# Optimization experiments

Measured on AMD Instinct MI355X. Metric: run time of the kernel, lower is better.

Reference implementation:

```python
import jax, jax.numpy as jnp
import numpy as np

N, E, G = 50000, 800000, 64
IN, ED = 2, 2
H1, C1 = 16, 8
H2, C2 = 4, 16
D1 = H1 * C1  # 128
D2 = H2 * C2  # 64


def _glorot(key, shape):
    fan_in, fan_out = shape[0], shape[-1]
    lim = jnp.sqrt(6.0 / (fan_in + fan_out))
    return jax.random.uniform(key, shape, jnp.float32, -lim, lim)


def setup_inputs() -> dict:
    key = jax.random.key(0)
    ks = jax.random.split(key, 16)
    x = jax.random.normal(ks[0], (N, IN), jnp.float32)
    edge_attr = jax.random.uniform(ks[1], (E, ED), jnp.float32)
    edge_index = jax.random.randint(ks[2], (2, E), 0, N, jnp.int64)
    batch = jnp.sort(jax.random.randint(ks[3], (N,), 0, G, jnp.int64))
    return {
        'x': x, 'edge_attr': edge_attr,
        'W_l1': _glorot(ks[4], (IN, D1)), 'b_l1': jnp.zeros((D1,), jnp.float32),
        'W_r1': _glorot(ks[5], (IN, D1)), 'b_r1': jnp.zeros((D1,), jnp.float32),
        'W_e1': _glorot(ks[6], (ED, D1)),
        'att1': _glorot(ks[7], (H1, C1)),
        'bias1': jnp.zeros((D1,), jnp.float32),
        'W_l2': _glorot(ks[8], (D1, D2)), 'b_l2': jnp.zeros((D2,), jnp.float32),
        'W_r2': _glorot(ks[9], (D1, D2)), 'b_r2': jnp.zeros((D2,), jnp.float32),
        'W_e2': _glorot(ks[10], (ED, D2)),
        'att2': _glorot(ks[11], (H2, C2)),
        'bias2': jnp.zeros((D2,), jnp.float32),
        'edge_index': edge_index, 'batch': batch,
    }


def _gatv2(x, edge_attr, src, tgt, Wl, bl, Wr, br, We, att, bias, H, C):
    n = x.shape[0]
    xl = (x @ Wl + bl).reshape(n, H, C)          # source transform (lin_l)
    xr = (x @ Wr + br).reshape(n, H, C)          # target transform (lin_r)
    xe = (edge_attr @ We).reshape(-1, H, C)      # edge transform (no bias)
    m = xl[src] + xr[tgt] + xe                   # [E,H,C]
    e = jnp.einsum('ehc,hc->eh', jax.nn.leaky_relu(m, 0.2), att)  # [E,H]
    emax = jax.ops.segment_max(e, tgt, num_segments=n)
    ee = jnp.exp(e - emax[tgt])
    denom = jax.ops.segment_sum(ee, tgt, num_segments=n)
    alpha = ee / denom[tgt]                      # segment softmax over in-edges
    out = jax.ops.segment_sum(alpha[:, :, None] * xl[src], tgt, num_segments=n)
    return out.reshape(n, H * C) + bias


def reference(x, edge_attr, W_l1, b_l1, W_r1, b_r1, W_e1, att1, bias1,
              W_l2, b_l2, W_r2, b_r2, W_e2, att2, bias2, edge_index, batch):
    src, tgt = edge_index[0], edge_index[1]
    h = _gatv2(x, edge_attr, src, tgt, W_l1, b_l1, W_r1, b_r1, W_e1, att1, bias1, H1, C1)
    h = jax.nn.elu(h)  # dropout is identity in eval mode
    h = _gatv2(h, edge_attr, src, tgt, W_l2, b_l2, W_r2, b_r2, W_e2, att2, bias2, H2, C2)
    # global_mean_pool over graphs
    sums = jax.ops.segment_sum(h, batch, num_segments=G)
    cnts = jax.ops.segment_sum(jnp.ones((h.shape[0], 1), h.dtype), batch, num_segments=G)
    return sums / jnp.maximum(cnts, 1.0)
```

## Files before the change

kernel.cpp:

```cpp
#include <hip/hip_runtime.h>
#include <math.h>

#define NBLK 256


template<int CTRL>
__device__ __forceinline__ float dppf(float x) {
    return __int_as_float(__builtin_amdgcn_update_dpp(
        0, __float_as_int(x), CTRL, 0xF, 0xF, true));
}
__device__ __forceinline__ float quadsum(float x) {
    x += dppf<0xB1>(x);
    x += dppf<0x4E>(x);
    return x;
}
__device__ __forceinline__ float sum16(float x) {
    x += dppf<0xB1>(x);
    x += dppf<0x4E>(x);
    x += dppf<0x141>(x);
    x += dppf<0x140>(x);
    return x;
}


__global__ __launch_bounds__(256) void k_hist(const int* __restrict__ tgt,
                                              int* __restrict__ gh,
                                              int e, int chunk, int nbuck) {
    __shared__ int lh[256];
    int tid = threadIdx.x, blk = blockIdx.x;
    lh[tid] = 0;
    __syncthreads();
    int lo = blk * chunk, hi = min(lo + chunk, e);
    for (int i = lo + tid; i < hi; i += 256)
        atomicAdd(&lh[tgt[i] >> 8], 1);
    __syncthreads();
    if (tid < nbuck) gh[tid * NBLK + blk] = lh[tid];
}


__global__ __launch_bounds__(256) void k_scanA(const int* __restrict__ deg,
                                               int* __restrict__ excl,
                                               int* __restrict__ bsum, int n) {
    int i = blockIdx.x * 256 + threadIdx.x;
    int lane = threadIdx.x & 63, wv = threadIdx.x >> 6;
    int v = (i < n) ? deg[i] : 0;
    int incl = v;
#pragma unroll
    for (int off = 1; off < 64; off <<= 1) {
        int t = __shfl_up(incl, off);
        if (lane >= off) incl += t;
    }
    __shared__ int ws[4];
    if (lane == 63) ws[wv] = incl;
    __syncthreads();
    int prefix = 0;
    for (int k = 0; k < wv; ++k) prefix += ws[k];
    if (i < n) excl[i] = prefix + incl - v;
    if (threadIdx.x == 255) bsum[blockIdx.x] = prefix + incl;
}

__global__ __launch_bounds__(256) void k_scanB(const int* __restrict__ bsum, int* __restrict__ boff,
                                               int* __restrict__ total_at, int nb, int n) {
    __shared__ int ws[4];
    __shared__ int carry_s;
    int lane = threadIdx.x & 63, wv = threadIdx.x >> 6;
    if (threadIdx.x == 0) carry_s = 0;
    __syncthreads();
    for (int base = 0; base < nb; base += 256) {
        int i = base + threadIdx.x;
        int v = (i < nb) ? bsum[i] : 0;
        int incl = v;
#pragma unroll
        for (int off = 1; off < 64; off <<= 1) {
            int t = __shfl_up(incl, off);
            if (lane >= off) incl += t;
        }
        if (lane == 63) ws[wv] = incl;
        __syncthreads();
        int prefix = carry_s;
        for (int k = 0; k < wv; ++k) prefix += ws[k];
        if (i < nb) boff[i] = prefix + incl - v;
        __syncthreads();
        if (threadIdx.x == 255) carry_s = prefix + incl;
        __syncthreads();
    }
    if (threadIdx.x == 0) total_at[n] = carry_s;
}

__global__ void k_scanC(int* __restrict__ arr, const int* __restrict__ boff, int n) {
    int i = blockIdx.x * 256 + threadIdx.x;
    if (i < n) arr[i] += boff[blockIdx.x];
}


__global__ __launch_bounds__(256) void k_binplace(const int* __restrict__ src,
                                                  const int* __restrict__ tgt,
                                                  const float* __restrict__ ea,
                                                  const float* __restrict__ x,
                                                  const int* __restrict__ gexcl,
                                                  float4* __restrict__ brec,
                                                  int* __restrict__ bmeta,
                                                  int e, int chunk, int nbuck) {
    __shared__ int loff[256];
    int tid = threadIdx.x, blk = blockIdx.x;
    if (tid < nbuck) loff[tid] = gexcl[tid * NBLK + blk];
    __syncthreads();
    int lo = blk * chunk, hi = min(lo + chunk, e);
    for (int i = lo + tid; i < hi; i += 256) {
        int t = tgt[i], s = src[i];
        float2 ev = ((const float2*)ea)[i];
        float2 xv = *(const float2*)(x + 2 * (size_t)s);
        int dst = atomicAdd(&loff[t >> 8], 1);
        brec[dst] = make_float4(xv.x, xv.y, ev.x, ev.y);
        bmeta[dst] = (s & 0xFFFF) | ((t & 0xFF) << 16);
    }
}


__global__ __launch_bounds__(256) void k_place2(const int* __restrict__ gexcl,
                                                const int* __restrict__ bmeta,
                                                const float4* __restrict__ brec,
                                                float4* __restrict__ col_rec,
                                                int* __restrict__ col_src,
                                                int* __restrict__ rowp, int n) {
    __shared__ int hist[256];
    __shared__ int pos[256];
    __shared__ int ws[4];
    int b = blockIdx.x, tid = threadIdx.x;
    int lo = gexcl[b * NBLK], hi = gexcl[(b + 1) * NBLK];
    hist[tid] = 0;
    __syncthreads();
    for (int i = lo + tid; i < hi; i += 256)
        atomicAdd(&hist[(bmeta[i] >> 16) & 0xFF], 1);
    __syncthreads();
    int lane = tid & 63, wv = tid >> 6;
    int v = hist[tid];
    int incl = v;
#pragma unroll
    for (int off = 1; off < 64; off <<= 1) {
        int t = __shfl_up(incl, off);
        if (lane >= off) incl += t;
    }
    if (lane == 63) ws[wv] = incl;
    __syncthreads();
    int prefix = 0;
    for (int k = 0; k < wv; ++k) prefix += ws[k];
    int rp = lo + prefix + incl - v;
    int node = b * 256 + tid;
    if (node <= n) rowp[node] = rp;
    if (b == (int)gridDim.x - 1 && tid == 0) rowp[n] = hi;
    pos[tid] = rp;
    __syncthreads();
    for (int i = lo + tid; i < hi; i += 256) {
        int m = bmeta[i];
        float4 r = brec[i];
        int slot = atomicAdd(&pos[(m >> 16) & 0xFF], 1);
        col_rec[slot] = r;
        col_src[slot] = m & 0xFFFF;
    }
}


__global__ __launch_bounds__(256) void k_agg1(
    const float* __restrict__ x,
    const int* __restrict__ rowp,
    const float4* __restrict__ col_rec,
    const float* __restrict__ W_l1, const float* __restrict__ b_l1,
    const float* __restrict__ W_r1, const float* __restrict__ b_r1,
    const float* __restrict__ W_e1,
    const float* __restrict__ att1,
    const float* __restrict__ bias1,
    float* __restrict__ hpost,
    int n)
{
    int wid = (blockIdx.x * blockDim.x + threadIdx.x) >> 6;
    if (wid >= n) return;
    int v = __builtin_amdgcn_readfirstlane(wid);
    int lane = threadIdx.x & 63;
    int f0 = 2 * lane, f1 = 2 * lane + 1;

    float Wl00 = W_l1[f0], Wl10 = W_l1[128 + f0], bl0 = b_l1[f0];
    float Wl01 = W_l1[f1], Wl11 = W_l1[128 + f1], bl1 = b_l1[f1];
    float We00 = W_e1[f0], We10 = W_e1[128 + f0];
    float We01 = W_e1[f1], We11 = W_e1[128 + f1];
    float a0 = att1[f0], a1 = att1[f1];

    float xv0 = x[2 * v], xv1 = x[2 * v + 1];
    float xrA = xv0 * W_r1[f0] + xv1 * W_r1[128 + f0] + b_r1[f0];
    float xrB = xv0 * W_r1[f1] + xv1 * W_r1[128 + f1] + b_r1[f1];

    float lh = 0.f, acc0 = 0.f, acc1 = 0.f;
    int rs = rowp[v], re = rowp[v + 1];
    bool b0 = (lane & 1) != 0, b1 = (lane & 2) != 0;

    int cs = rs;
#define E1(K, R) \
    float xa##K = fmaf(R.x, Wl00, fmaf(R.y, Wl10, bl0)); \
    float xb##K = fmaf(R.x, Wl01, fmaf(R.y, Wl11, bl1)); \
    float s##K; { \
        float m0 = xa##K + xrA + R.z * We00 + R.w * We10; \
        float m1 = xb##K + xrB + R.z * We01 + R.w * We11; \
        s##K = quadsum(fmaf(fmaxf(m0, 0.2f * m0), a0, fmaxf(m1, 0.2f * m1) * a1)); \
    }
    for (; cs + 4 <= re; cs += 4) {
        float4 r0 = col_rec[cs + 0];
        float4 r1 = col_rec[cs + 1];
        float4 r2 = col_rec[cs + 2];
        float4 r3 = col_rec[cs + 3];
        E1(0, r0) E1(1, r1) E1(2, r2) E1(3, r3)
        float sel01 = b0 ? s1 : s0;
        float sel23 = b0 ? s3 : s2;
        float smy = b1 ? sel23 : sel01;
        float p = __expf(smy);
        float p0 = dppf<0x00>(p), p1 = dppf<0x55>(p), p2 = dppf<0xAA>(p), p3 = dppf<0xFF>(p);
        lh += (p0 + p1) + (p2 + p3);
        acc0 += fmaf(p0, xa0, p1 * xa1) + fmaf(p2, xa2, p3 * xa3);
        acc1 += fmaf(p0, xb0, p1 * xb1) + fmaf(p2, xb2, p3 * xb3);
    }
#undef E1
    for (; cs < re; ++cs) {
        float4 r = col_rec[cs];
        float xa = fmaf(r.x, Wl00, fmaf(r.y, Wl10, bl0));
        float xb = fmaf(r.x, Wl01, fmaf(r.y, Wl11, bl1));
        float m0 = xa + xrA + r.z * We00 + r.w * We10;
        float m1 = xb + xrB + r.z * We01 + r.w * We11;
        float s = quadsum(fmaf(fmaxf(m0, 0.2f * m0), a0, fmaxf(m1, 0.2f * m1) * a1));
        float p = __expf(s);
        lh += p;
        acc0 = fmaf(p, xa, acc0);
        acc1 = fmaf(p, xb, acc1);
    }

    float r0o, r1o;
    if (re > rs) { float inv = 1.f / lh; r0o = acc0 * inv; r1o = acc1 * inv; }
    else { r0o = 0.f; r1o = 0.f; }
    r0o += bias1[f0]; r1o += bias1[f1];
    r0o = (r0o > 0.f) ? r0o : (__expf(r0o) - 1.f);
    r1o = (r1o > 0.f) ? r1o : (__expf(r1o) - 1.f);
    *(float2*)(hpost + (size_t)v * 128 + f0) = make_float2(r0o, r1o);
}


struct XF2Shared {
    float4 hs[64 * 32];
    float4 ws[128 * 16];
};

__device__ __forceinline__ void xf2_pass(XF2Shared& sm,
                                         const float* __restrict__ W,
                                         const float* __restrict__ b,
                                         float* __restrict__ out,
                                         int v0, int n, int t) {
    __syncthreads();
    {
        const float4* wsrc = (const float4*)W;
#pragma unroll
        for (int i = 0; i < 8; ++i) sm.ws[t + 256 * i] = wsrc[t + 256 * i];
    }
    __syncthreads();

    int lane = t & 63, w = t >> 6;
    int fg = lane & 3, ng = lane >> 2;
    int fq = 4 * w + fg;
    int hsw = ng & 7;

    float acc[4][4];
#pragma unroll
    for (int i = 0; i < 4; ++i)
#pragma unroll
        for (int c = 0; c < 4; ++c) acc[i][c] = 0.f;

    for (int kq = 0; kq < 32; ++kq) {
        float4 w0 = sm.ws[(4 * kq + 0) * 16 + fq];
        float4 w1 = sm.ws[(4 * kq + 1) * 16 + fq];
        float4 w2 = sm.ws[(4 * kq + 2) * 16 + fq];
        float4 w3 = sm.ws[(4 * kq + 3) * 16 + fq];
        int ks = kq ^ hsw;
        float4 h0 = sm.hs[(4 * ng + 0) * 32 + ks];
        float4 h1 = sm.hs[(4 * ng + 1) * 32 + ks];
        float4 h2 = sm.hs[(4 * ng + 2) * 32 + ks];
        float4 h3 = sm.hs[(4 * ng + 3) * 32 + ks];
#pragma unroll
        for (int i = 0; i < 4; ++i) {
            float4 h = (i == 0) ? h0 : (i == 1) ? h1 : (i == 2) ? h2 : h3;
            acc[i][0] += h.x * w0.x; acc[i][1] += h.x * w0.y; acc[i][2] += h.x * w0.z; acc[i][3] += h.x * w0.w;
            acc[i][0] += h.y * w1.x; acc[i][1] += h.y * w1.y; acc[i][2] += h.y * w1.z; acc[i][3] += h.y * w1.w;
            acc[i][0] += h.z * w2.x; acc[i][1] += h.z * w2.y; acc[i][2] += h.z * w2.z; acc[i][3] += h.z * w2.w;
            acc[i][0] += h.w * w3.x; acc[i][1] += h.w * w3.y; acc[i][2] += h.w * w3.z; acc[i][3] += h.w * w3.w;
        }
    }

    float4 bf = ((const float4*)b)[fq];
#pragma unroll
    for (int i = 0; i < 4; ++i) {
        int node = v0 + 4 * ng + i;
        if (node < n) {
            float4 r = make_float4(acc[i][0] + bf.x, acc[i][1] + bf.y,
                                   acc[i][2] + bf.z, acc[i][3] + bf.w);
            *(float4*)(out + (size_t)node * 64 + 4 * fq) = r;
        }
    }
}

__global__ __launch_bounds__(256) void k_transform2(
    const float* __restrict__ hpost,
    const float* __restrict__ W_l2, const float* __restrict__ b_l2,
    const float* __restrict__ W_r2, const float* __restrict__ b_r2,
    float* __restrict__ xl2, float* __restrict__ xr2, int n)
{
    __shared__ XF2Shared sm;
    int t = threadIdx.x;
    int v0 = blockIdx.x * 64;
    {
        int node = t >> 2, sub = t & 3;
        int sw = (node >> 2) & 7;
        bool valid = (v0 + node) < n;
        const float4* src = (const float4*)(hpost + (size_t)(v0 + node) * 128);
#pragma unroll
        for (int i = 0; i < 8; ++i) {
            int kq = sub + 4 * i;
            float4 val = valid ? src[kq] : make_float4(0.f, 0.f, 0.f, 0.f);
            sm.hs[node * 32 + (kq ^ sw)] = val;
        }
    }
    xf2_pass(sm, W_l2, b_l2, xl2, v0, n, t);
    xf2_pass(sm, W_r2, b_r2, xr2, v0, n, t);
}


__global__ __launch_bounds__(256) void k_agg2(
    const float* __restrict__ xl2,
    const float* __restrict__ xr2,
    const int* __restrict__ rowp,
    const int* __restrict__ col_src,
    const float4* __restrict__ col_rec,
    const float* __restrict__ W_e2,
    const float* __restrict__ att2,
    const float* __restrict__ bias2,
    float* __restrict__ h2,
    int n)
{
    int wid = (blockIdx.x * blockDim.x + threadIdx.x) >> 6;
    if (wid >= n) return;
    int v = __builtin_amdgcn_readfirstlane(wid);
    int lane = threadIdx.x & 63;
    float We0 = W_e2[lane], We1 = W_e2[64 + lane];
    float a = att2[lane];
    float xr = xr2[(size_t)v * 64 + lane];
    float lh = 0.f, acc = 0.f;
    int rs = rowp[v], re = rowp[v + 1];
    const float2* eap = (const float2*)col_rec;
    bool b0 = (lane & 1) != 0, b1 = (lane & 2) != 0;

    int cs = rs;
#define E2(K, EV, XL) \
    float s##K; { \
        float m = XL + xr + EV.x * We0 + EV.y * We1; \
        s##K = sum16(fmaxf(m, 0.2f * m) * a); \
    }
    for (; cs + 4 <= re; cs += 4) {
        int u0 = col_src[cs], u1 = col_src[cs + 1], u2 = col_src[cs + 2], u3 = col_src[cs + 3];
        float2 e0 = eap[2 * cs + 1], e1 = eap[2 * cs + 3];
        float2 e2 = eap[2 * cs + 5], e3 = eap[2 * cs + 7];
        float xl0 = xl2[(size_t)u0 * 64 + lane];
        float xl1 = xl2[(size_t)u1 * 64 + lane];
        float xl2_ = xl2[(size_t)u2 * 64 + lane];
        float xl3 = xl2[(size_t)u3 * 64 + lane];
        E2(0, e0, xl0) E2(1, e1, xl1) E2(2, e2, xl2_) E2(3, e3, xl3)
        float sel01 = b0 ? s1 : s0;
        float sel23 = b0 ? s3 : s2;
        float smy = b1 ? sel23 : sel01;
        float p = __expf(smy);
        float p0 = dppf<0x00>(p), p1 = dppf<0x55>(p), p2 = dppf<0xAA>(p), p3 = dppf<0xFF>(p);
        lh += (p0 + p1) + (p2 + p3);
        acc += fmaf(p0, xl0, p1 * xl1) + fmaf(p2, xl2_, p3 * xl3);
    }
#undef E2
    for (; cs < re; ++cs) {
        int u = col_src[cs];
        float2 ev = eap[2 * cs + 1];
        float xl = xl2[(size_t)u * 64 + lane];
        float m = xl + xr + ev.x * We0 + ev.y * We1;
        float s = sum16(fmaxf(m, 0.2f * m) * a);
        float p = __expf(s);
        lh += p;
        acc = fmaf(p, xl, acc);
    }
    float r = (re > rs) ? acc / lh : 0.f;
    h2[(size_t)v * 64 + lane] = r + bias2[lane];
}


__global__ __launch_bounds__(256) void k_pool2(const float* __restrict__ h2,
                                               const int* __restrict__ batch,
                                               float* __restrict__ sums, float* __restrict__ cnt,
                                               int n, int chunk) {
    int w = (blockIdx.x * blockDim.x + threadIdx.x) >> 6;
    int lane = threadIdx.x & 63;
    int start = w * chunk;
    if (start >= n) return;
    int end = min(n, start + chunk);
    int g = batch[start];
    float acc = 0.f;
    int c = 0;
    for (int v = start; v < end; ++v) {
        int bg = batch[v];
        if (bg != g) {
            atomicAdd(&sums[g * 64 + lane], acc);
            if (lane == 0) atomicAdd(&cnt[g], (float)c);
            acc = 0.f; c = 0; g = bg;
        }
        acc += h2[(size_t)v * 64 + lane];
        ++c;
    }
    atomicAdd(&sums[g * 64 + lane], acc);
    if (lane == 0) atomicAdd(&cnt[g], (float)c);
}

__global__ void k_final(const float* __restrict__ sums, const float* __restrict__ cnt,
                        float* __restrict__ out, int g) {
    int i = blockIdx.x * blockDim.x + threadIdx.x;
    if (i < g * 64) out[i] = sums[i] / fmaxf(cnt[i >> 6], 1.f);
}


extern "C" void kernel_launch(void* const* d_in, const int* in_sizes, int n_in,
                              void* d_out, int out_size, void* d_ws, size_t ws_size,
                              hipStream_t stream) {
    const float* x     = (const float*)d_in[0];
    const float* ea    = (const float*)d_in[1];
    const float* W_l1  = (const float*)d_in[2];
    const float* b_l1  = (const float*)d_in[3];
    const float* W_r1  = (const float*)d_in[4];
    const float* b_r1  = (const float*)d_in[5];
    const float* W_e1  = (const float*)d_in[6];
    const float* att1  = (const float*)d_in[7];
    const float* bias1 = (const float*)d_in[8];
    const float* W_l2  = (const float*)d_in[9];
    const float* b_l2  = (const float*)d_in[10];
    const float* W_r2  = (const float*)d_in[11];
    const float* b_r2  = (const float*)d_in[12];
    const float* W_e2  = (const float*)d_in[13];
    const float* att2  = (const float*)d_in[14];
    const float* bias2 = (const float*)d_in[15];
    const int* eidx    = (const int*)d_in[16];
    const int* batch   = (const int*)d_in[17];

    int n = in_sizes[0] / 2;
    int e = in_sizes[16] / 2;
    int g = out_size / 64;
    const int* srcI = eidx;
    const int* tgtI = eidx + e;
    int nb = (n + 255) / 256;
    int ntot = nb * NBLK;
    int nb2 = (ntot + 255) / 256;
    int chunk = (e + NBLK - 1) / NBLK;

    char* w = (char*)d_ws;
    size_t off = 0;
    auto take = [&](size_t bytes) -> char* {
        size_t a = (off + 255) & ~(size_t)255;
        off = a + bytes;
        return w + a;
    };
    char*   reg1    = take((size_t)n * 128 * 4);
    float4* brec    = (float4*)reg1;
    float*  hpost   = (float*)reg1;
    float*  h2      = hpost;
    char*   reg2    = take((size_t)n * 64 * 4);
    int*    bmeta   = (int*)reg2;
    float*  xl2     = (float*)reg2;

    float*  xr2     = (float*)take((size_t)n * 64 * 4);
    float4* col_rec = (float4*)take((size_t)e * 16);
    int*    col_src = (int*)take((size_t)e * 4);
    int*    rowp    = (int*)take((size_t)(n + 1) * 4);
    int*    gh      = (int*)take((size_t)ntot * 4);
    int*    gexcl   = (int*)take((size_t)(ntot + 1) * 4);
    int*    gbsum   = (int*)take((size_t)nb2 * 4);
    int*    gboff   = (int*)take((size_t)nb2 * 4);
    float*  sums    = (float*)take((size_t)g * 64 * 4);
    float*  cnt     = (float*)take((size_t)g * 4);

    hipMemsetAsync(sums, 0, (size_t)g * 64 * 4, stream);
    hipMemsetAsync(cnt, 0, (size_t)g * 4, stream);

    k_hist<<<NBLK, 256, 0, stream>>>(tgtI, gh, e, chunk, nb);
    k_scanA<<<nb2, 256, 0, stream>>>(gh, gexcl, gbsum, ntot);
    k_scanB<<<1, 256, 0, stream>>>(gbsum, gboff, gexcl, nb2, ntot);
    k_scanC<<<nb2, 256, 0, stream>>>(gexcl, gboff, ntot);
    k_binplace<<<NBLK, 256, 0, stream>>>(srcI, tgtI, ea, x, gexcl, brec, bmeta, e, chunk, nb);
    k_place2<<<nb, 256, 0, stream>>>(gexcl, bmeta, brec, col_rec, col_src, rowp, n);

    int nwaveblocks = (n * 64 + 255) / 256;
    k_agg1<<<nwaveblocks, 256, 0, stream>>>(x, rowp, col_rec,
                                            W_l1, b_l1, W_r1, b_r1, W_e1, att1, bias1,
                                            hpost, n);
    int ntiles = (n + 63) / 64;
    k_transform2<<<ntiles, 256, 0, stream>>>(hpost, W_l2, b_l2, W_r2, b_r2, xl2, xr2, n);
    k_agg2<<<nwaveblocks, 256, 0, stream>>>(xl2, xr2, rowp, col_src, col_rec,
                                            W_e2, att2, bias2, h2, n);

    int pool_waves = 1024;
    int pool_chunk = (n + pool_waves - 1) / pool_waves;
    k_pool2<<<pool_waves / 4, 256, 0, stream>>>(h2, batch, sums, cnt, n, pool_chunk);
    k_final<<<(g * 64 + 255) / 256, 256, 0, stream>>>(sums, cnt, (float*)d_out, g);
}
```

Measured before the change: 186.7 us.

## Fold scan fixup into consumers, persistent-grid aggregation, kernel memset, more binning blocks

Removes the k_scanC pass by adding the per-block scan offset where the prefix is read in binplace and place2. Replaces two memsets with one init kernel. The aggregation kernels become grid-stride loops over fixed 1024-block grids, so weights and biases are loaded once per wave instead of once per node. NBLK is doubled to 512 so binning uses more blocks. The accumulation order is changed to chained FMAs, which slightly alters rounding and lengthens the dependency chain.

Measured after the change: 207.6 us. +11.2%, slower.

```diff
diff --git a/kernel.cpp b/kernel.cpp
--- a/kernel.cpp
+++ b/kernel.cpp
@@ -1,7 +1,7 @@
 #include <hip/hip_runtime.h>
 #include <math.h>
 
-#define NBLK 256
+#define NBLK 512
 
 
 template<int CTRL>
@@ -20,6 +20,13 @@
     x += dppf<0x141>(x);
     x += dppf<0x140>(x);
     return x;
+}
+
+
+__global__ void k_init(float* __restrict__ sums, float* __restrict__ cnt, int gn) {
+    int i = blockIdx.x * 256 + threadIdx.x;
+    if (i < gn * 64) sums[i] = 0.f;
+    if (i < gn) cnt[i] = 0.f;
 }
 
 
@@ -60,7 +67,7 @@
 }
 
 __global__ __launch_bounds__(256) void k_scanB(const int* __restrict__ bsum, int* __restrict__ boff,
-                                               int* __restrict__ total_at, int nb, int n) {
+                                               int nb) {
     __shared__ int ws[4];
     __shared__ int carry_s;
     int lane = threadIdx.x & 63, wv = threadIdx.x >> 6;
@@ -84,12 +91,6 @@
         if (threadIdx.x == 255) carry_s = prefix + incl;
         __syncthreads();
     }
-    if (threadIdx.x == 0) total_at[n] = carry_s;
-}
-
-__global__ void k_scanC(int* __restrict__ arr, const int* __restrict__ boff, int n) {
-    int i = blockIdx.x * 256 + threadIdx.x;
-    if (i < n) arr[i] += boff[blockIdx.x];
 }
 
 
@@ -98,12 +99,16 @@
                                                   const float* __restrict__ ea,
                                                   const float* __restrict__ x,
                                                   const int* __restrict__ gexcl,
+                                                  const int* __restrict__ gboff,
                                                   float4* __restrict__ brec,
                                                   int* __restrict__ bmeta,
                                                   int e, int chunk, int nbuck) {
     __shared__ int loff[256];
     int tid = threadIdx.x, blk = blockIdx.x;
-    if (tid < nbuck) loff[tid] = gexcl[tid * NBLK + blk];
+    if (tid < nbuck) {
+        int cell = tid * NBLK + blk;
+        loff[tid] = gexcl[cell] + gboff[cell >> 8];
+    }
     __syncthreads();
     int lo = blk * chunk, hi = min(lo + chunk, e);
     for (int i = lo + tid; i < hi; i += 256) {
@@ -118,16 +123,20 @@
 
 
 __global__ __launch_bounds__(256) void k_place2(const int* __restrict__ gexcl,
+                                                const int* __restrict__ gboff,
                                                 const int* __restrict__ bmeta,
                                                 const float4* __restrict__ brec,
                                                 float4* __restrict__ col_rec,
                                                 int* __restrict__ col_src,
-                                                int* __restrict__ rowp, int n) {
+                                                int* __restrict__ rowp,
+                                                int n, int ntot, int e) {
     __shared__ int hist[256];
     __shared__ int pos[256];
     __shared__ int ws[4];
     int b = blockIdx.x, tid = threadIdx.x;
-    int lo = gexcl[b * NBLK], hi = gexcl[(b + 1) * NBLK];
+    int clo = b * NBLK, chi = clo + NBLK;
+    int lo = gexcl[clo] + gboff[clo >> 8];
+    int hi = (chi >= ntot) ? e : (gexcl[chi] + gboff[chi >> 8]);
     hist[tid] = 0;
     __syncthreads();
     for (int i = lo + tid; i < hi; i += 256)
@@ -173,71 +182,73 @@
     float* __restrict__ hpost,
     int n)
 {
-    int wid = (blockIdx.x * blockDim.x + threadIdx.x) >> 6;
-    if (wid >= n) return;
-    int v = __builtin_amdgcn_readfirstlane(wid);
     int lane = threadIdx.x & 63;
-    int f0 = 2 * lane, f1 = 2 * lane + 1;
-
+    int f0 = 2 * lane, f1 = f0 + 1;
     float Wl00 = W_l1[f0], Wl10 = W_l1[128 + f0], bl0 = b_l1[f0];
     float Wl01 = W_l1[f1], Wl11 = W_l1[128 + f1], bl1 = b_l1[f1];
     float We00 = W_e1[f0], We10 = W_e1[128 + f0];
     float We01 = W_e1[f1], We11 = W_e1[128 + f1];
     float a0 = att1[f0], a1 = att1[f1];
-
-    float xv0 = x[2 * v], xv1 = x[2 * v + 1];
-    float xrA = xv0 * W_r1[f0] + xv1 * W_r1[128 + f0] + b_r1[f0];
-    float xrB = xv0 * W_r1[f1] + xv1 * W_r1[128 + f1] + b_r1[f1];
-
-    float lh = 0.f, acc0 = 0.f, acc1 = 0.f;
-    int rs = rowp[v], re = rowp[v + 1];
+    float Wr00 = W_r1[f0], Wr10 = W_r1[128 + f0], br0 = b_r1[f0];
+    float Wr01 = W_r1[f1], Wr11 = W_r1[128 + f1], br1 = b_r1[f1];
+    float bs0 = bias1[f0], bs1 = bias1[f1];
     bool b0 = (lane & 1) != 0, b1 = (lane & 2) != 0;
-
-    int cs = rs;
+    int nw = (int)gridDim.x << 2;
+    int v = __builtin_amdgcn_readfirstlane(((int)blockIdx.x << 2) | (threadIdx.x >> 6));
+
+    for (; v < n; v += nw) {
+        float xv0 = x[2 * v], xv1 = x[2 * v + 1];
+        float xrA = fmaf(xv0, Wr00, fmaf(xv1, Wr10, br0));
+        float xrB = fmaf(xv0, Wr01, fmaf(xv1, Wr11, br1));
+        float lh = 0.f, acc0 = 0.f, acc1 = 0.f;
+        int rs = rowp[v], re = rowp[v + 1];
+        int cs = rs;
 #define E1(K, R) \
-    float xa##K = fmaf(R.x, Wl00, fmaf(R.y, Wl10, bl0)); \
-    float xb##K = fmaf(R.x, Wl01, fmaf(R.y, Wl11, bl1)); \
-    float s##K; { \
-        float m0 = xa##K + xrA + R.z * We00 + R.w * We10; \
-        float m1 = xb##K + xrB + R.z * We01 + R.w * We11; \
-        s##K = quadsum(fmaf(fmaxf(m0, 0.2f * m0), a0, fmaxf(m1, 0.2f * m1) * a1)); \
-    }
-    for (; cs + 4 <= re; cs += 4) {
-        float4 r0 = col_rec[cs + 0];
-        float4 r1 = col_rec[cs + 1];
-        float4 r2 = col_rec[cs + 2];
-        float4 r3 = col_rec[cs + 3];
-        E1(0, r0) E1(1, r1) E1(2, r2) E1(3, r3)
-        float sel01 = b0 ? s1 : s0;
-        float sel23 = b0 ? s3 : s2;
-        float smy = b1 ? sel23 : sel01;
-        float p = __expf(smy);
-        float p0 = dppf<0x00>(p), p1 = dppf<0x55>(p), p2 = dppf<0xAA>(p), p3 = dppf<0xFF>(p);
-        lh += (p0 + p1) + (p2 + p3);
-        acc0 += fmaf(p0, xa0, p1 * xa1) + fmaf(p2, xa2, p3 * xa3);
-        acc1 += fmaf(p0, xb0, p1 * xb1) + fmaf(p2, xb2, p3 * xb3);
-    }
+        float xa##K = fmaf(R.x, Wl00, fmaf(R.y, Wl10, bl0)); \
+        float xb##K = fmaf(R.x, Wl01, fmaf(R.y, Wl11, bl1)); \
+        float s##K; { \
+            float m0 = xa##K + xrA + R.z * We00 + R.w * We10; \
+            float m1 = xb##K + xrB + R.z * We01 + R.w * We11; \
+            s##K = quadsum(fmaf(fmaxf(m0, 0.2f * m0), a0, fmaxf(m1, 0.2f * m1) * a1)); \
+        }
+        for (; cs + 4 <= re; cs += 4) {
+            float4 r0 = col_rec[cs + 0];
+            float4 r1 = col_rec[cs + 1];
+            float4 r2 = col_rec[cs + 2];
+            float4 r3 = col_rec[cs + 3];
+            E1(0, r0) E1(1, r1) E1(2, r2) E1(3, r3)
+            float sel01 = b0 ? s1 : s0;
+            float sel23 = b0 ? s3 : s2;
+            float smy = b1 ? sel23 : sel01;
+            float p = __expf(smy);
+            float p0 = dppf<0x00>(p), p1 = dppf<0x55>(p), p2 = dppf<0xAA>(p), p3 = dppf<0xFF>(p);
+            lh += quadsum(p);
+            acc0 = fmaf(p0, xa0, acc0); acc0 = fmaf(p1, xa1, acc0);
+            acc0 = fmaf(p2, xa2, acc0); acc0 = fmaf(p3, xa3, acc0);
+            acc1 = fmaf(p0, xb0, acc1); acc1 = fmaf(p1, xb1, acc1);
+            acc1 = fmaf(p2, xb2, acc1); acc1 = fmaf(p3, xb3, acc1);
+        }
 #undef E1
-    for (; cs < re; ++cs) {
-        float4 r = col_rec[cs];
-        float xa = fmaf(r.x, Wl00, fmaf(r.y, Wl10, bl0));
-        float xb = fmaf(r.x, Wl01, fmaf(r.y, Wl11, bl1));
-        float m0 = xa + xrA + r.z * We00 + r.w * We10;
-        float m1 = xb + xrB + r.z * We01 + r.w * We11;
-        float s = quadsum(fmaf(fmaxf(m0, 0.2f * m0), a0, fmaxf(m1, 0.2f * m1) * a1));
-        float p = __expf(s);
-        lh += p;
-        acc0 = fmaf(p, xa, acc0);
-        acc1 = fmaf(p, xb, acc1);
-    }
-
-    float r0o, r1o;
-    if (re > rs) { float inv = 1.f / lh; r0o = acc0 * inv; r1o = acc1 * inv; }
-    else { r0o = 0.f; r1o = 0.f; }
-    r0o += bias1[f0]; r1o += bias1[f1];
-    r0o = (r0o > 0.f) ? r0o : (__expf(r0o) - 1.f);
-    r1o = (r1o > 0.f) ? r1o : (__expf(r1o) - 1.f);
-    *(float2*)(hpost + (size_t)v * 128 + f0) = make_float2(r0o, r1o);
+        for (; cs < re; ++cs) {
+            float4 r = col_rec[cs];
+            float xa = fmaf(r.x, Wl00, fmaf(r.y, Wl10, bl0));
+            float xb = fmaf(r.x, Wl01, fmaf(r.y, Wl11, bl1));
+            float m0 = xa + xrA + r.z * We00 + r.w * We10;
+            float m1 = xb + xrB + r.z * We01 + r.w * We11;
+            float s = quadsum(fmaf(fmaxf(m0, 0.2f * m0), a0, fmaxf(m1, 0.2f * m1) * a1));
+            float p = __expf(s);
+            lh += p;
+            acc0 = fmaf(p, xa, acc0);
+            acc1 = fmaf(p, xb, acc1);
+        }
+        float r0o, r1o;
+        if (re > rs) { float inv = 1.f / lh; r0o = acc0 * inv; r1o = acc1 * inv; }
+        else { r0o = 0.f; r1o = 0.f; }
+        r0o += bs0; r1o += bs1;
+        r0o = (r0o > 0.f) ? r0o : (__expf(r0o) - 1.f);
+        r1o = (r1o > 0.f) ? r1o : (__expf(r1o) - 1.f);
+        *(float2*)(hpost + (size_t)v * 128 + f0) = make_float2(r0o, r1o);
+    }
 }
 
 
@@ -340,54 +351,57 @@
     float* __restrict__ h2,
     int n)
 {
-    int wid = (blockIdx.x * blockDim.x + threadIdx.x) >> 6;
-    if (wid >= n) return;
-    int v = __builtin_amdgcn_readfirstlane(wid);
     int lane = threadIdx.x & 63;
     float We0 = W_e2[lane], We1 = W_e2[64 + lane];
     float a = att2[lane];
-    float xr = xr2[(size_t)v * 64 + lane];
-    float lh = 0.f, acc = 0.f;
-    int rs = rowp[v], re = rowp[v + 1];
+    float bs = bias2[lane];
+    bool b0 = (lane & 1) != 0, b1 = (lane & 2) != 0;
     const float2* eap = (const float2*)col_rec;
-    bool b0 = (lane & 1) != 0, b1 = (lane & 2) != 0;
-
-    int cs = rs;
+    int nw = (int)gridDim.x << 2;
+    int v = __builtin_amdgcn_readfirstlane(((int)blockIdx.x << 2) | (threadIdx.x >> 6));
+
+    for (; v < n; v += nw) {
+        float xr = xr2[(size_t)v * 64 + lane];
+        float lh = 0.f, acc = 0.f;
+        int rs = rowp[v], re = rowp[v + 1];
+        int cs = rs;
 #define E2(K, EV, XL) \
-    float s##K; { \
-        float m = XL + xr + EV.x * We0 + EV.y * We1; \
-        s##K = sum16(fmaxf(m, 0.2f * m) * a); \
-    }
-    for (; cs + 4 <= re; cs += 4) {
-        int u0 = col_src[cs], u1 = col_src[cs + 1], u2 = col_src[cs + 2], u3 = col_src[cs + 3];
-        float2 e0 = eap[2 * cs + 1], e1 = eap[2 * cs + 3];
-        float2 e2 = eap[2 * cs + 5], e3 = eap[2 * cs + 7];
-        float xl0 = xl2[(size_t)u0 * 64 + lane];
-        float xl1 = xl2[(size_t)u1 * 64 + lane];
-        float xl2_ = xl2[(size_t)u2 * 64 + lane];
-        float xl3 = xl2[(size_t)u3 * 64 + lane];
-        E2(0, e0, xl0) E2(1, e1, xl1) E2(2, e2, xl2_) E2(3, e3, xl3)
-        float sel01 = b0 ? s1 : s0;
-        float sel23 = b0 ? s3 : s2;
-        float smy = b1 ? sel23 : sel01;
-        float p = __expf(smy);
-        float p0 = dppf<0x00>(p), p1 = dppf<0x55>(p), p2 = dppf<0xAA>(p), p3 = dppf<0xFF>(p);
-        lh += (p0 + p1) + (p2 + p3);
-        acc += fmaf(p0, xl0, p1 * xl1) + fmaf(p2, xl2_, p3 * xl3);
-    }
+        float s##K; { \
+            float m = XL + xr + EV.x * We0 + EV.y * We1; \
+            s##K = sum16(fmaxf(m, 0.2f * m) * a); \
+        }
+        for (; cs + 4 <= re; cs += 4) {
+            int u0 = col_src[cs], u1 = col_src[cs + 1], u2 = col_src[cs + 2], u3 = col_src[cs + 3];
+            float2 e0 = eap[2 * cs + 1], e1 = eap[2 * cs + 3];
+            float2 e2 = eap[2 * cs + 5], e3 = eap[2 * cs + 7];
+            float xl0 = xl2[(size_t)u0 * 64 + lane];
+            float xl1 = xl2[(size_t)u1 * 64 + lane];
+            float xl2_ = xl2[(size_t)u2 * 64 + lane];
+            float xl3 = xl2[(size_t)u3 * 64 + lane];
+            E2(0, e0, xl0) E2(1, e1, xl1) E2(2, e2, xl2_) E2(3, e3, xl3)
+            float sel01 = b0 ? s1 : s0;
+            float sel23 = b0 ? s3 : s2;
+            float smy = b1 ? sel23 : sel01;
+            float p = __expf(smy);
+            float p0 = dppf<0x00>(p), p1 = dppf<0x55>(p), p2 = dppf<0xAA>(p), p3 = dppf<0xFF>(p);
+            lh += quadsum(p);
+            acc = fmaf(p0, xl0, acc); acc = fmaf(p1, xl1, acc);
+            acc = fmaf(p2, xl2_, acc); acc = fmaf(p3, xl3, acc);
+        }
 #undef E2
-    for (; cs < re; ++cs) {
-        int u = col_src[cs];
-        float2 ev = eap[2 * cs + 1];
-        float xl = xl2[(size_t)u * 64 + lane];
-        float m = xl + xr + ev.x * We0 + ev.y * We1;
-        float s = sum16(fmaxf(m, 0.2f * m) * a);
-        float p = __expf(s);
-        lh += p;
-        acc = fmaf(p, xl, acc);
-    }
-    float r = (re > rs) ? acc / lh : 0.f;
-    h2[(size_t)v * 64 + lane] = r + bias2[lane];
+        for (; cs < re; ++cs) {
+            int u = col_src[cs];
+            float2 ev = eap[2 * cs + 1];
+            float xl = xl2[(size_t)u * 64 + lane];
+            float m = xl + xr + ev.x * We0 + ev.y * We1;
+            float s = sum16(fmaxf(m, 0.2f * m) * a);
+            float p = __expf(s);
+            lh += p;
+            acc = fmaf(p, xl, acc);
+        }
+        float r = (re > rs) ? acc / lh : 0.f;
+        h2[(size_t)v * 64 + lane] = r + bs;
+    }
 }
 
 
@@ -482,24 +496,23 @@
     float*  sums    = (float*)take((size_t)g * 64 * 4);
     float*  cnt     = (float*)take((size_t)g * 4);
 
-    hipMemsetAsync(sums, 0, (size_t)g * 64 * 4, stream);
-    hipMemsetAsync(cnt, 0, (size_t)g * 4, stream);
+    k_init<<<(g * 64 + 255) / 256, 256, 0, stream>>>(sums, cnt, g);
 
     k_hist<<<NBLK, 256, 0, stream>>>(tgtI, gh, e, chunk, nb);
     k_scanA<<<nb2, 256, 0, stream>>>(gh, gexcl, gbsum, ntot);
-    k_scanB<<<1, 256, 0, stream>>>(gbsum, gboff, gexcl, nb2, ntot);
-    k_scanC<<<nb2, 256, 0, stream>>>(gexcl, gboff, ntot);
-    k_binplace<<<NBLK, 256, 0, stream>>>(srcI, tgtI, ea, x, gexcl, brec, bmeta, e, chunk, nb);
-    k_place2<<<nb, 256, 0, stream>>>(gexcl, bmeta, brec, col_rec, col_src, rowp, n);
-
-    int nwaveblocks = (n * 64 + 255) / 256;
-    k_agg1<<<nwaveblocks, 256, 0, stream>>>(x, rowp, col_rec,
-                                            W_l1, b_l1, W_r1, b_r1, W_e1, att1, bias1,
-                                            hpost, n);
+    k_scanB<<<1, 256, 0, stream>>>(gbsum, gboff, nb2);
+    k_binplace<<<NBLK, 256, 0, stream>>>(srcI, tgtI, ea, x, gexcl, gboff, brec, bmeta,
+                                         e, chunk, nb);
+    k_place2<<<nb, 256, 0, stream>>>(gexcl, gboff, bmeta, brec, col_rec, col_src, rowp,
+                                     n, ntot, e);
+
+    k_agg1<<<1024, 256, 0, stream>>>(x, rowp, col_rec,
+                                     W_l1, b_l1, W_r1, b_r1, W_e1, att1, bias1,
+                                     hpost, n);
     int ntiles = (n + 63) / 64;
     k_transform2<<<ntiles, 256, 0, stream>>>(hpost, W_l2, b_l2, W_r2, b_r2, xl2, xr2, n);
-    k_agg2<<<nwaveblocks, 256, 0, stream>>>(xl2, xr2, rowp, col_src, col_rec,
-                                            W_e2, att2, bias2, h2, n);
+    k_agg2<<<1024, 256, 0, stream>>>(xl2, xr2, rowp, col_src, col_rec,
+                                     W_e2, att2, bias2, h2, n);
 
     int pool_waves = 1024;
     int pool_chunk = (n + pool_waves - 1) / pool_waves;
```
